# Kernel tuning notes

Hardware: AMD Instinct MI355X
Metric: run time of the kernel (lower is better)

The kernel has to match this reference:

```python
import jax, jax.numpy as jnp
import numpy as np

# Dimensions
B, C, H, W = 4, 256, 64, 64
O = 256                      # out_channels
K = 3                        # kernel size
K2 = K * K
STRIDE = (1, 1)
PAD = 1
Ho = (H + 2 * PAD - K) // STRIDE[0] + 1   # 64
Wo = (W + 2 * PAD - K) // STRIDE[1] + 1   # 64


def setup_inputs() -> dict:
    key = jax.random.key(0)
    ks = jax.random.split(key, 5)
    x = jax.random.normal(ks[0], (B, C, H, W), jnp.float32)
    # NOTE: the torch module zero-inits offset/modulator convs; we use small
    # random weights so the deformable sampling path is actually exercised.
    offset_w = 0.02 * jax.random.normal(ks[1], (2 * K2, C, K, K), jnp.float32)
    offset_b = jnp.zeros((2 * K2,), jnp.float32)
    mod_w = 0.02 * jax.random.normal(ks[2], (K2, C, K, K), jnp.float32)
    mod_b = jnp.zeros((K2,), jnp.float32)
    weight = jax.random.normal(ks[3], (O, C, K, K), jnp.float32) / np.sqrt(C * K2)
    return {"x": x, "offset_w": offset_w, "offset_b": offset_b,
            "mod_w": mod_w, "mod_b": mod_b, "weight": weight}


def _conv(x, w, b):
    y = jax.lax.conv_general_dilated(
        x, w, window_strides=STRIDE, padding=[(PAD, PAD), (PAD, PAD)],
        dimension_numbers=("NCHW", "OIHW", "NCHW"))
    return y + b[None, :, None, None]


def _deform_conv2d(x, offset, mask, weight):
    """Modulated deformable conv v2 (torchvision semantics, zero padding)."""
    Bq, Cq, Hq, Wq = x.shape
    # offset channels are (dy, dx) pairs per kernel tap, row-major over kernel
    off = offset.reshape(Bq, K2, 2, Ho, Wo)
    ky, kx = jnp.meshgrid(jnp.arange(K), jnp.arange(K), indexing="ij")
    ky = ky.reshape(K2).astype(x.dtype)
    kx = kx.reshape(K2).astype(x.dtype)
    hy = (jnp.arange(Ho) * STRIDE[0] - PAD).astype(x.dtype)
    wx = (jnp.arange(Wo) * STRIDE[1] - PAD).astype(x.dtype)
    # sampling positions [B, K2, Ho, Wo]
    py = off[:, :, 0] + ky[None, :, None, None] + hy[None, None, :, None]
    px = off[:, :, 1] + kx[None, :, None, None] + wx[None, None, None, :]

    P = K2 * Ho * Wo
    xf = x.reshape(Bq, Cq, Hq * Wq)
    y0 = jnp.floor(py)
    x0 = jnp.floor(px)
    val = jnp.zeros((Bq, Cq, P), x.dtype)
    for dy in (0.0, 1.0):
        for dx in (0.0, 1.0):
            yc = y0 + dy
            xc = x0 + dx
            wgt = (1.0 - jnp.abs(py - yc)) * (1.0 - jnp.abs(px - xc))
            valid = (yc >= 0) & (yc < Hq) & (xc >= 0) & (xc < Wq)
            idx = (jnp.clip(yc, 0, Hq - 1) * Wq
                   + jnp.clip(xc, 0, Wq - 1)).astype(jnp.int32).reshape(Bq, P)
            g = jnp.take_along_axis(xf, idx[:, None, :], axis=2)  # [B,C,P]
            val = val + (wgt * valid.astype(x.dtype)).reshape(Bq, 1, P) * g
    # modulation mask is per kernel tap, shared across channels
    cols = (val * mask.reshape(Bq, 1, P)).reshape(Bq, Cq, K2, Ho * Wo)
    out = jnp.einsum("bckp,ock->bop", cols, weight.reshape(weight.shape[0], Cq, K2))
    return out.reshape(Bq, weight.shape[0], Ho, Wo)


def reference(x, offset_w, offset_b, mod_w, mod_b, weight):
    offset = _conv(x, offset_w, offset_b)
    mask = 2.0 * jax.nn.sigmoid(_conv(x, mod_w, mod_b))
    return _deform_conv2d(x, offset, mask, weight)
```

## Files before the change

kernel.cpp:

```cpp
#include <hip/hip_runtime.h>
#include <math.h>


constexpr int Bn = 4;
constexpr int Cn = 256;
constexpr int Hn = 64;
constexpr int Wn = 64;
constexpr int On = 256;
constexpr int PB = Hn * Wn;
constexpr int NCH = 27;

typedef __attribute__((ext_vector_type(8))) _Float16 f16x8;
typedef __attribute__((ext_vector_type(2))) _Float16 f16x2;
typedef __attribute__((ext_vector_type(4))) float f32x4;
typedef __attribute__((ext_vector_type(4))) uint  uint4v;

union FragU { uint4 u; f16x8 h; };

__device__ inline ushort f2h(float f) {
    _Float16 h = (_Float16)f;
    return __builtin_bit_cast(ushort, h);
}
__device__ inline uint pkh(float a, float b) {
    return __builtin_bit_cast(uint, __builtin_amdgcn_cvt_pkrtz(a, b));
}
__device__ inline f16x2 u2h(uint u) { return __builtin_bit_cast(f16x2, u); }
__device__ inline uint h2u(f16x2 h) { return __builtin_bit_cast(uint, h); }

__global__ __launch_bounds__(256)
void nhwcpack_kernel(const float* __restrict__ x,
                     const float* __restrict__ w,
                     const float* __restrict__ offw,
                     const float* __restrict__ modw,
                     ushort* __restrict__ xhf,
                     ushort* __restrict__ wTb,
                     ushort* __restrict__ owf)
{
    const int bid = blockIdx.x;
    const int b = bid >> 7, seg = bid & 127;
    const int t = threadIdx.x;
    __shared__ float tile2[256][36];

    {
        const int c0 = t >> 3;
        const int q  = t & 7;
        const float* src = x + (size_t)b * Cn * PB + seg * 32 + 4 * q;
        #pragma unroll
        for (int i = 0; i < 8; ++i) {
            const int c = c0 + i * 32;
            const float4 v = *reinterpret_cast<const float4*>(src + (size_t)c * PB);
            *reinterpret_cast<float4*>(&tile2[c][4 * q]) = v;
        }
    }
    __syncthreads();

    {
        const int c2 = t & 127;
        const int ph = t >> 7;
        uint* dH = reinterpret_cast<uint*>(xhf + ((size_t)b * PB + seg * 32) * 256);
        #pragma unroll
        for (int r = 0; r < 2; ++r) {
            const int ppb = (ph + 2 * r) * 8;
            const float4 a0 = *reinterpret_cast<const float4*>(&tile2[2 * c2][ppb]);
            const float4 a1 = *reinterpret_cast<const float4*>(&tile2[2 * c2][ppb + 4]);
            const float4 b0 = *reinterpret_cast<const float4*>(&tile2[2 * c2 + 1][ppb]);
            const float4 b1 = *reinterpret_cast<const float4*>(&tile2[2 * c2 + 1][ppb + 4]);
            uint wds[8];
            wds[0] = pkh(a0.x, b0.x); wds[1] = pkh(a0.y, b0.y);
            wds[2] = pkh(a0.z, b0.z); wds[3] = pkh(a0.w, b0.w);
            wds[4] = pkh(a1.x, b1.x); wds[5] = pkh(a1.y, b1.y);
            wds[6] = pkh(a1.z, b1.z); wds[7] = pkh(a1.w, b1.w);
            #pragma unroll
            for (int j = 0; j < 8; ++j)
                dH[(size_t)(ppb + j) * 128 + c2] = wds[j];
        }
    }

    #pragma unroll 1
    for (int u = 0; u < 5; ++u) {
        int unit = (u < 4) ? bid * 4 + u : (bid < 256 ? 2048 + bid : -1);
        if (unit < 0) break;
        const int tap = unit >> 8, c = unit & 255;
        const int o = t;
        wTb[((size_t)(unit >> 3) * 256 + o) * 8 + (c & 7)] =
            f2h(w[((size_t)o * Cn + c) * 9 + tap]);
        if (o < 32) {
            float v = 0.f;
            if (o < 18)      v = offw[((size_t)o * Cn + c) * 9 + tap];
            else if (o < 27) v = modw[((size_t)(o - 18) * Cn + c) * 9 + tap];
            owf[((size_t)(unit >> 3) * 32 + o) * 8 + (c & 7)] = f2h(v);
        }
    }
}

__global__ __launch_bounds__(512, 1)
void offmask_tile_kernel(const ushort* __restrict__ xhf,
                         const float* __restrict__ offb,
                         const float* __restrict__ modb,
                         const ushort* __restrict__ owf,
                         float* __restrict__ offm)
{
    const int hw = blockIdx.x;
    const int blk = (hw & 7) * 32 + (hw >> 3);
    const int b = blk >> 6, row = blk & 63;
    const int t = threadIdx.x;
    const int lane = t & 63;
    const int wv  = t >> 6;
    const int l15 = lane & 15;
    const int g   = lane >> 4;
    const int mt  = wv >> 2;
    const int nt  = wv & 3;

    __shared__ ushort xt[3 * 66 * 256];
    uint4* lds4 = reinterpret_cast<uint4*>(xt);

    {
        const int c  = t >> 3;
        const int og = (t & 7) * 4;
        #pragma unroll 1
        for (int r = 0; r < 3; ++r) {
            const int ysrc = row - 1 + r;
            const int ci = c + 1;
            const int base = (r * 66 + ci) * 32;
            if (ysrc >= 0 && ysrc < Hn) {
                const uint4* src = reinterpret_cast<const uint4*>(
                    xhf + ((size_t)(b * PB + ysrc * 64 + c)) * 256);
                #pragma unroll
                for (int j = 0; j < 4; ++j) {
                    const int o = og + j;
                    lds4[base + (o ^ (ci & 7))] = src[o];
                }
            } else {
                const uint4 z = make_uint4(0u, 0u, 0u, 0u);
                #pragma unroll
                for (int j = 0; j < 4; ++j) {
                    const int o = og + j;
                    lds4[base + (o ^ (ci & 7))] = z;
                }
            }
        }
        if (t < 192) {
            const int r = t >> 6, idx = t & 63;
            const int ci = (idx >= 32) ? 65 : 0;
            const int o = idx & 31;
            lds4[(r * 66 + ci) * 32 + (o ^ (ci & 7))] =
                make_uint4(0u, 0u, 0u, 0u);
        }
    }
    __syncthreads();

    const uint4* owfV = reinterpret_cast<const uint4*>(owf);
    f32x4 acc = (f32x4){0.f, 0.f, 0.f, 0.f};
    const int pos = nt * 16 + l15;

    #pragma unroll 1
    for (int tap = 0; tap < 9; ++tap) {
        const int ty = tap / 3, tx = tap % 3;
        const int ci = pos + tx;
        const int cbase = (ty * 66 + ci) * 32;
        const int cx = ci & 7;

        uint4 aH[8];
        #pragma unroll
        for (int s = 0; s < 8; ++s) {
            const size_t kb = (size_t)((tap * 8 + s) * 4 + g) * 32 + mt * 16 + l15;
            aH[s] = owfV[kb];
        }

        #pragma unroll
        for (int s = 0; s < 8; ++s) {
            FragU aHH, bH;
            aHH.u = aH[s];
            bH.u = lds4[cbase + ((4 * s + g) ^ cx)];
            acc = __builtin_amdgcn_mfma_f32_16x16x32_f16(aHH.h, bH.h, acc, 0, 0, 0);
        }
    }

    #pragma unroll
    for (int j = 0; j < 4; ++j) {
        const int ch = mt * 16 + g * 4 + j;
        if (ch < NCH) {
            float v = acc[j];
            if (ch < 18) v += offb[ch];
            else         v = 2.f / (1.f + expf(-(v + modb[ch - 18])));
            offm[((size_t)(b * NCH + ch)) * PB + row * 64 + pos] = v;
        }
    }
}

__global__ __launch_bounds__(1024, 1)
void deform_ws_kernel(const ushort* __restrict__ xhf,
                      const float* __restrict__ offm,
                      const ushort* __restrict__ wTb,
                      float* __restrict__ out)
{
    const int hw = blockIdx.x;
    const int blk = (hw & 7) * 32 + (hw >> 3);
    const int b = blk >> 6, row = blk & 63;
    const int p0 = row * 64;
    const int t = threadIdx.x;
    const int lane = t & 63;
    const int wv  = t >> 6;
    const int l15 = lane & 15;
    const int g   = lane >> 4;

    __shared__ int4  s_off[576];
    __shared__ uint4 s_wgt[576];
    __shared__ uint  cols[2][4][1024];

    for (int ti = t; ti < 576; ti += 1024) {
        const int k = ti >> 6, pos = ti & 63;
        const int p = p0 + pos;
        const float dy = offm[((size_t)(b * NCH + 2 * k)) * PB + p];
        const float dx = offm[((size_t)(b * NCH + 2 * k + 1)) * PB + p];
        const float m  = offm[((size_t)(b * NCH + 18 + k)) * PB + p];
        const int ky = k / 3, kx = k % 3;
        const float py = dy + (float)(ky + row - 1);
        const float px = dx + (float)(kx + pos - 1);
        const float y0f = floorf(py), x0f = floorf(px);
        const float fy = py - y0f, fx = px - x0f;
        const int y0 = (int)y0f, x0i = (int)x0f;
        const int y1 = y0 + 1, x1 = x0i + 1;
        const bool vy0 = (y0 >= 0) && (y0 < Hn);
        const bool vy1 = (y1 >= 0) && (y1 < Hn);
        const bool vx0 = (x0i >= 0) && (x0i < Wn);
        const bool vx1 = (x1 >= 0) && (x1 < Wn);
        const int y0c = min(max(y0, 0), Hn - 1);
        const int y1c = min(max(y1, 0), Hn - 1);
        const int x0c = min(max(x0i, 0), Wn - 1);
        const int x1c = min(max(x1, 0), Wn - 1);
        s_off[ti] = make_int4(y0c * Wn + x0c, y0c * Wn + x1c,
                              y1c * Wn + x0c, y1c * Wn + x1c);
        const float w0 = (vy0 && vx0) ? (1.f - fy) * (1.f - fx) * m : 0.f;
        const float w1 = (vy0 && vx1) ? (1.f - fy) * fx * m : 0.f;
        const float w2 = (vy1 && vx0) ? fy * (1.f - fx) * m : 0.f;
        const float w3 = (vy1 && vx1) ? fy * fx * m : 0.f;
        s_wgt[ti] = make_uint4(pkh(w0, w0), pkh(w1, w1),
                               pkh(w2, w2), pkh(w3, w3));
    }
    __syncthreads();

    const ushort* xb = xhf + (size_t)b * PB * 256;

    if (wv < 8) {
        const int chq  = t & 15;
        const int posT = t >> 4;
        const int sIdx = chq >> 2;
        const int grp  = (chq & 3) ^ (posT & 3) ^ ((posT >> 2) & 3);
        const int w4a  = posT * 4 + grp;
        const ushort* xq = xb + 8 * chq;

        auto PISSUE = [&](int cch, uint4v (&gg)[2][4]) {
            const int tap = cch >> 1;
            const ushort* xcc = xq + (cch & 1) * 128;
            #pragma unroll
            for (int u = 0; u < 2; ++u) {
                const int4 o = s_off[tap * 64 + posT + u * 32];
                gg[u][0] = *reinterpret_cast<const uint4v*>(xcc + (size_t)o.x * 256);
                gg[u][1] = *reinterpret_cast<const uint4v*>(xcc + (size_t)o.y * 256);
                gg[u][2] = *reinterpret_cast<const uint4v*>(xcc + (size_t)o.z * 256);
                gg[u][3] = *reinterpret_cast<const uint4v*>(xcc + (size_t)o.w * 256);
            }
        };

        auto PCOMBINE = [&](int cch, const uint4v (&gg)[2][4], uint* cbuf) {
            const int tap = cch >> 1;
            uint4v* dst = reinterpret_cast<uint4v*>(cbuf + sIdx * 1024);
            #pragma unroll
            for (int u = 0; u < 2; ++u) {
                const uint4 wq = s_wgt[tap * 64 + posT + u * 32];
                uint pr[4];
                #pragma unroll
                for (int j = 0; j < 4; ++j) {
                    f16x2 v = u2h(gg[u][0][j]) * u2h(wq.x);
                    v += u2h(gg[u][1][j]) * u2h(wq.y);
                    v += u2h(gg[u][2][j]) * u2h(wq.z);
                    v += u2h(gg[u][3][j]) * u2h(wq.w);
                    pr[j] = h2u(v);
                }
                dst[w4a + u * 128] = (uint4v){pr[0], pr[1], pr[2], pr[3]};
            }
        };

        uint4v gA[2][4], gB[2][4];
        PISSUE(0, gA);
        #pragma unroll 1
        for (int jj = 0; jj < 9; ++jj) {
            PISSUE(2 * jj + 1, gB);
            PCOMBINE(2 * jj, gA, &cols[0][0][0]);
            asm volatile("s_waitcnt lgkmcnt(0)" ::: "memory");
            __builtin_amdgcn_s_barrier();
            asm volatile("" ::: "memory");
            if (jj < 8) PISSUE(2 * jj + 2, gA);
            PCOMBINE(2 * jj + 1, gB, &cols[1][0][0]);
            asm volatile("s_waitcnt lgkmcnt(0)" ::: "memory");
            __builtin_amdgcn_s_barrier();
            asm volatile("" ::: "memory");
        }
    } else {
        const int cw = wv - 8;
        const int o0 = cw * 32;
        const uint4* wvp = reinterpret_cast<const uint4*>(wTb);

        int ri[4];
        #pragma unroll
        for (int nt = 0; nt < 4; ++nt) {
            const int p = nt * 16 + l15;
            ri[nt] = p * 4 + (g ^ (p & 3) ^ ((p >> 2) & 3));
        }

        f32x4 acc[2][4];
        #pragma unroll
        for (int i = 0; i < 2; ++i)
            #pragma unroll
            for (int nt = 0; nt < 4; ++nt)
                acc[i][nt] = (f32x4){0.f, 0.f, 0.f, 0.f};

        auto CLOADA = [&](int cch, uint4 (&ap)[4][2]) {
            #pragma unroll
            for (int s = 0; s < 4; ++s) {
                const int kb = (cch * 4 + s) * 4 + g;
                ap[s][0] = wvp[(size_t)kb * 256 + o0 + l15];
                ap[s][1] = wvp[(size_t)kb * 256 + o0 + 16 + l15];
            }
        };

        auto CMFMA = [&](const uint* cbuf, const uint4 (&ap)[4][2]) {
            __builtin_amdgcn_s_setprio(1);
            #pragma unroll
            for (int s = 0; s < 4; ++s) {
                FragU a0, a1, bf[4];
                a0.u = ap[s][0]; a1.u = ap[s][1];
                #pragma unroll
                for (int nt = 0; nt < 4; ++nt)
                    bf[nt].u = reinterpret_cast<const uint4*>(cbuf + s * 1024)[ri[nt]];
                #pragma unroll
                for (int nt = 0; nt < 4; ++nt) {
                    acc[0][nt] = __builtin_amdgcn_mfma_f32_16x16x32_f16(
                        a0.h, bf[nt].h, acc[0][nt], 0, 0, 0);
                    acc[1][nt] = __builtin_amdgcn_mfma_f32_16x16x32_f16(
                        a1.h, bf[nt].h, acc[1][nt], 0, 0, 0);
                }
            }
            __builtin_amdgcn_s_setprio(0);
        };

        uint4 aA[4][2], aB[4][2];
        CLOADA(0, aA);
        #pragma unroll 1
        for (int jj = 0; jj < 9; ++jj) {
            __builtin_amdgcn_s_barrier();
            asm volatile("" ::: "memory");
            CLOADA(2 * jj + 1, aB);
            CMFMA(&cols[0][0][0], aA);
            __builtin_amdgcn_s_barrier();
            asm volatile("" ::: "memory");
            if (jj < 8) CLOADA(2 * jj + 2, aA);
            CMFMA(&cols[1][0][0], aB);
        }

        float* ob = out + (size_t)b * On * PB;
        #pragma unroll
        for (int i = 0; i < 2; ++i)
            #pragma unroll
            for (int nt = 0; nt < 4; ++nt)
                #pragma unroll
                for (int j = 0; j < 4; ++j)
                    ob[((size_t)(o0 + i * 16 + g * 4 + j)) * PB
                       + p0 + nt * 16 + l15] = acc[i][nt][j];
    }
}

extern "C" void kernel_launch(void* const* d_in, const int* in_sizes, int n_in,
                              void* d_out, int out_size, void* d_ws, size_t ws_size,
                              hipStream_t stream)
{
    const float* x    = (const float*)d_in[0];
    const float* offw = (const float*)d_in[1];
    const float* offb = (const float*)d_in[2];
    const float* modw = (const float*)d_in[3];
    const float* modb = (const float*)d_in[4];
    const float* wgt  = (const float*)d_in[5];
    float* out = (float*)d_out;

    char* ws = (char*)d_ws;
    float*  offm = (float*)ws;
    ushort* wTb  = (ushort*)(ws + 1769472);
    ushort* owf  = (ushort*)(ws + 2949120);
    ushort* xhf  = (ushort*)(ws + 3244032);

    nhwcpack_kernel<<<dim3(512), dim3(256), 0, stream>>>(
        x, wgt, offw, modw, xhf, wTb, owf);
    offmask_tile_kernel<<<dim3(256), dim3(512), 0, stream>>>(
        xhf, offb, modb, owf, offm);
    deform_ws_kernel<<<dim3(256), dim3(1024), 0, stream>>>(
        xhf, offm, wTb, out);
}
```

Measured before the change: 56.15 us.

## Deepen LDS ring to six stages, syncing once per three chunks

The column buffer in LDS grows from two slots to six, so producer waves fill three chunks before each barrier and consumer waves run MFMA over three chunks between barriers. This cuts the number of workgroup barriers in the producer/consumer pipeline by a factor of three and lets the two sides drift further apart. In exchange LDS use rises to about 96KB for cols, and the A-fragment prefetch schedule grows more complex.

```diff
diff --git a/kernel.cpp b/kernel.cpp
--- a/kernel.cpp
+++ b/kernel.cpp
@@ -206,7 +206,7 @@
 
     __shared__ int4  s_off[576];
     __shared__ uint4 s_wgt[576];
-    __shared__ uint  cols[2][4][1024];
+    __shared__ uint  cols[6][4][1024];
 
     for (int ti = t; ti < 576; ti += 1024) {
         const int k = ti >> 6, pos = ti & 63;
@@ -285,14 +285,23 @@
         uint4v gA[2][4], gB[2][4];
         PISSUE(0, gA);
         #pragma unroll 1
-        for (int jj = 0; jj < 9; ++jj) {
-            PISSUE(2 * jj + 1, gB);
-            PCOMBINE(2 * jj, gA, &cols[0][0][0]);
+        for (int mi = 0; mi < 3; ++mi) {
+            const int c0 = 6 * mi;
+            PISSUE(c0 + 1, gB);
+            PCOMBINE(c0, gA, &cols[0][0][0]);
+            PISSUE(c0 + 2, gA);
+            PCOMBINE(c0 + 1, gB, &cols[1][0][0]);
+            PISSUE(c0 + 3, gB);
+            PCOMBINE(c0 + 2, gA, &cols[2][0][0]);
             asm volatile("s_waitcnt lgkmcnt(0)" ::: "memory");
             __builtin_amdgcn_s_barrier();
             asm volatile("" ::: "memory");
-            if (jj < 8) PISSUE(2 * jj + 2, gA);
-            PCOMBINE(2 * jj + 1, gB, &cols[1][0][0]);
+            PISSUE(c0 + 4, gA);
+            PCOMBINE(c0 + 3, gB, &cols[3][0][0]);
+            PISSUE(c0 + 5, gB);
+            PCOMBINE(c0 + 4, gA, &cols[4][0][0]);
+            if (mi < 2) PISSUE(c0 + 6, gA);
+            PCOMBINE(c0 + 5, gB, &cols[5][0][0]);
             asm volatile("s_waitcnt lgkmcnt(0)" ::: "memory");
             __builtin_amdgcn_s_barrier();
             asm volatile("" ::: "memory");
@@ -347,16 +356,26 @@
 
         uint4 aA[4][2], aB[4][2];
         CLOADA(0, aA);
+        CLOADA(1, aB);
         #pragma unroll 1
-        for (int jj = 0; jj < 9; ++jj) {
+        for (int mi = 0; mi < 3; ++mi) {
+            const int c0 = 6 * mi;
             __builtin_amdgcn_s_barrier();
             asm volatile("" ::: "memory");
-            CLOADA(2 * jj + 1, aB);
             CMFMA(&cols[0][0][0], aA);
+            CLOADA(c0 + 2, aA);
+            CMFMA(&cols[1][0][0], aB);
+            CLOADA(c0 + 3, aB);
+            CMFMA(&cols[2][0][0], aA);
+            CLOADA(c0 + 4, aA);
             __builtin_amdgcn_s_barrier();
             asm volatile("" ::: "memory");
-            if (jj < 8) CLOADA(2 * jj + 2, aA);
-            CMFMA(&cols[1][0][0], aB);
+            CMFMA(&cols[3][0][0], aB);
+            CLOADA(c0 + 5, aB);
+            CMFMA(&cols[4][0][0], aA);
+            if (mi < 2) CLOADA(c0 + 6, aA);
+            CMFMA(&cols[5][0][0], aB);
+            if (mi < 2) CLOADA(c0 + 7, aB);
         }
 
         float* ob = out + (size_t)b * On * PB;
```

New measurement: 53.80 us. 4.2% less time.
